# Optimization experiments

Hardware: AMD Instinct MI355X
Metric: run time of the kernel (lower is better)

The kernel has to match this reference:

```python
import jax, jax.numpy as jnp
import numpy as np

N_NODES = 100000
N_EDGES = 600000
EMB_DIM = 128
N_BOND_FEATS = 3
BOND_VOCAB = 8


def setup_inputs() -> dict:
    key = jax.random.key(0)
    k1, k2, k3, k4, k5, k6 = jax.random.split(key, 6)
    h = jax.random.normal(k1, (N_NODES, EMB_DIM), dtype=jnp.float32)
    edge_feat = jax.random.randint(k2, (N_EDGES, N_BOND_FEATS), 0, 5, dtype=jnp.int64)
    dst = jax.random.randint(k3, (N_EDGES,), 0, N_NODES, dtype=jnp.int64)
    bond_emb = jax.random.normal(k4, (N_BOND_FEATS, BOND_VOCAB, EMB_DIM), dtype=jnp.float32)
    W = jax.random.normal(k5, (EMB_DIM, EMB_DIM), dtype=jnp.float32) / jnp.sqrt(jnp.float32(EMB_DIM))
    b = jax.random.normal(k6, (EMB_DIM,), dtype=jnp.float32) * 0.01
    return {"h": h, "edge_feat": edge_feat, "dst": dst, "bond_emb": bond_emb, "W": W, "b": b}


def reference(h, edge_feat, dst, bond_emb, W, b):
    # BondEncoder: sum of per-column embedding lookups -> [E, D]
    # bond_emb[f, edge_feat[:, f]] for each feature column f, summed.
    he = bond_emb[jnp.arange(N_BOND_FEATS)[None, :], edge_feat].sum(axis=1)  # [E, D]
    # fn.v_mul_e: message = dst-node feature * encoded edge feature
    m = h[dst] * he  # [E, D]
    # fn.sum: segment-sum messages onto destination nodes
    agg = jax.ops.segment_sum(m, dst, num_segments=N_NODES)  # [N, D]
    # final Linear(emb_dim, emb_dim)
    return agg @ W.T + b
```

## Files before the change

### kernel.cpp

```cpp
#include <hip/hip_runtime.h>

#define NN 100000
#define NE 600000
#define D 128
#define CW 16

#define OFF_CNTBF  6400000
#define OFF_WSPLIT 9600000
#define OFF_EFRAG  9665536

typedef __attribute__((ext_vector_type(8))) short bf16x8;
typedef __attribute__((ext_vector_type(4))) float f32x4;

__device__ __forceinline__ unsigned short f2bf(float x) {
    unsigned u = __float_as_uint(x);
    u += 0x7FFFu + ((u >> 16) & 1u);
    return (unsigned short)(u >> 16);
}
__device__ __forceinline__ float bf2f(unsigned short s) {
    return __uint_as_float(((unsigned)s) << 16);
}
__device__ __forceinline__ unsigned pack2(unsigned short a, unsigned short b) {
    return (unsigned)a | ((unsigned)b << 16);
}

__global__ __launch_bounds__(256) void prep_kernel(const float* __restrict__ W,
                                                   const float* __restrict__ emb,
                                                   unsigned char* __restrict__ ws) {
    int bid = blockIdx.x;
    if (bid < 1563) {
        int c = bid * 256 + threadIdx.x;
        if (c < 400000) reinterpret_cast<int4*>(ws)[c] = make_int4(0, 0, 0, 0);
    } else if (bid < 1627) {
        int idx = (bid - 1563) * 256 + threadIdx.x;
        float w = W[idx];
        unsigned short hi = f2bf(w);
        unsigned short lo = f2bf(w - bf2f(hi));
        unsigned short* wsplit = (unsigned short*)(ws + OFF_WSPLIT);
        wsplit[idx] = hi;
        wsplit[16384 + idx] = lo;
    } else {
        int i = (bid - 1627) * 256 + threadIdx.x;
        int e = i & 7, l = (i >> 3) & 63, t = (i >> 9) & 7;
        int r = l & 15, lg = l >> 4;
        int j = lg * 8 + e;
        int d = 32 * (t >> 1) + 8 * (r >> 2) + 4 * (t & 1) + (r & 3);
        float v = 0.0f;
        if (j < 15) v = emb[((j / 5) * 8 + (j % 5)) * D + d];
        unsigned short hi = f2bf(v);
        unsigned short lo = f2bf(v - bf2f(hi));
        unsigned short* ef = (unsigned short*)(ws + OFF_EFRAG);
        ef[i] = hi;
        ef[4096 + i] = lo;
    }
}

__global__ __launch_bounds__(256) void hist_kernel(const int* __restrict__ ef,
                                                   const int* __restrict__ dst,
                                                   unsigned* __restrict__ counts) {
    int g = blockIdx.x * 256 + threadIdx.x;
    if (g >= NE / 4) return;
    int4 d4 = reinterpret_cast<const int4*>(dst)[g];
    int4 f0 = reinterpret_cast<const int4*>(ef)[g * 3 + 0];
    int4 f1 = reinterpret_cast<const int4*>(ef)[g * 3 + 1];
    int4 f2 = reinterpret_cast<const int4*>(ef)[g * 3 + 2];
    int fa[12] = {f0.x, f0.y, f0.z, f0.w, f1.x, f1.y, f1.z, f1.w,
                  f2.x, f2.y, f2.z, f2.w};
    int dd[4] = {d4.x, d4.y, d4.z, d4.w};
    #pragma unroll
    for (int i = 0; i < 4; ++i) {
        int combo = fa[i * 3] * 25 + fa[i * 3 + 1] * 5 + fa[i * 3 + 2];
        atomicAdd(counts + dd[i] * CW + (combo >> 3), 1u << ((combo & 7) * 4));
    }
}

__global__ __launch_bounds__(256) void expand_kernel(const unsigned* __restrict__ counts,
                                                     unsigned short* __restrict__ cntbf) {
    int n = blockIdx.x * 256 + threadIdx.x;
    if (n >= NN) return;
    const unsigned* row = counts + n * CW;
    unsigned wd[16];
    #pragma unroll
    for (int i = 0; i < 4; ++i) {
        uint4 v = reinterpret_cast<const uint4*>(row)[i];
        wd[i * 4] = v.x; wd[i * 4 + 1] = v.y; wd[i * 4 + 2] = v.z; wd[i * 4 + 3] = v.w;
    }
    int mi[15];
    #pragma unroll
    for (int j = 0; j < 15; ++j) mi[j] = 0;
    #pragma unroll
    for (int c = 0; c < 125; ++c) {
        int cnt = (int)((wd[c >> 3] >> ((c & 7) * 4)) & 0xFu);
        mi[c / 25] += cnt;
        mi[5 + (c / 5) % 5] += cnt;
        mi[10 + c % 5] += cnt;
    }
    unsigned short o[16];
    #pragma unroll
    for (int j = 0; j < 15; ++j) o[j] = f2bf((float)mi[j]);
    o[15] = 0;
    uint4 u;
    u.x = pack2(o[0], o[1]);   u.y = pack2(o[2], o[3]);
    u.z = pack2(o[4], o[5]);   u.w = pack2(o[6], o[7]);
    reinterpret_cast<uint4*>(cntbf + n * 16)[0] = u;
    u.x = pack2(o[8], o[9]);   u.y = pack2(o[10], o[11]);
    u.z = pack2(o[12], o[13]); u.w = pack2(o[14], o[15]);
    reinterpret_cast<uint4*>(cntbf + n * 16)[1] = u;
}

__global__ __launch_bounds__(512, 4) void fused_kernel(
        const float* __restrict__ h,
        const unsigned short* __restrict__ cntbf,
        const unsigned short* __restrict__ efrag,
        const unsigned short* __restrict__ wsplit,
        const float* __restrict__ b,
        float* __restrict__ out) {
    __shared__ unsigned short sW[2][128 * 128];
    __shared__ unsigned short sA[64 * 128];

    const int tid  = threadIdx.x;
    const int lane = tid & 63;
    const int w    = tid >> 6;
    const int n0   = blockIdx.x * 64;
    const int lr   = lane & 15;
    const int lg   = lane >> 4;

    char* sWb = (char*)&sW[0][0];
    char* sAb = (char*)&sA[0];

    #pragma unroll
    for (int i = 0; i < 8; ++i) {
        int c  = tid + i * 512;
        int p  = c >> 11;
        int r  = (c >> 4) & 127;
        int kc = c & 15;
        int byte = p * 32768 + r * 256 + ((kc * 16) ^ ((r & 7) << 4));
        *reinterpret_cast<uint4*>(sWb + byte) = reinterpret_cast<const uint4*>(wsplit)[c];
    }

    const int ng   = w & 3;
    const int th   = w >> 2;
    const int node = n0 + ng * 16 + lr;
    const bool valid = node < NN;

    bf16x8 cfrag = {0, 0, 0, 0, 0, 0, 0, 0};
    if (valid && lg < 2)
        cfrag = *reinterpret_cast<const bf16x8*>(cntbf + node * 16 + lg * 8);

    f32x4 s[4];
    #pragma unroll
    for (int ti = 0; ti < 4; ++ti) { f32x4 z = {0, 0, 0, 0}; s[ti] = z; }
    #pragma unroll
    for (int p = 0; p < 2; ++p) {
        #pragma unroll
        for (int ti = 0; ti < 4; ++ti) {
            int t = th * 4 + ti;
            bf16x8 ef = *reinterpret_cast<const bf16x8*>(efrag + p * 4096 + t * 512 + lane * 8);
            s[ti] = __builtin_amdgcn_mfma_f32_16x16x32_bf16(ef, cfrag, s[ti], 0, 0, 0);
        }
    }

    #pragma unroll
    for (int q = 0; q < 2; ++q) {
        const int u = th * 2 + q;
        float hv[8];
        if (valid) {
            float4 h0 = *reinterpret_cast<const float4*>(h + node * D + u * 32 + lg * 8);
            float4 h1 = *reinterpret_cast<const float4*>(h + node * D + u * 32 + lg * 8 + 4);
            hv[0] = h0.x; hv[1] = h0.y; hv[2] = h0.z; hv[3] = h0.w;
            hv[4] = h1.x; hv[5] = h1.y; hv[6] = h1.z; hv[7] = h1.w;
        } else {
            #pragma unroll
            for (int e = 0; e < 8; ++e) hv[e] = 0.0f;
        }
        unsigned short o[8];
        #pragma unroll
        for (int e = 0; e < 8; ++e)
            o[e] = f2bf(hv[e] * s[q * 2 + (e >> 2)][e & 3]);
        uint4 uo;
        uo.x = pack2(o[0], o[1]); uo.y = pack2(o[2], o[3]);
        uo.z = pack2(o[4], o[5]); uo.w = pack2(o[6], o[7]);
        int row  = ng * 16 + lr;
        int byte = row * 256 + ((u * 64 + lg * 16) ^ ((row & 7) << 4));
        *reinterpret_cast<uint4*>(sAb + byte) = uo;
    }
    __syncthreads();

    const int mt = w >> 1;
    const int jc = w & 1;

    f32x4 acc[4];
    #pragma unroll
    for (int jb = 0; jb < 4; ++jb) {
        float bv = b[jc * 64 + jb * 16 + lr];
        f32x4 t = {bv, bv, bv, bv};
        acc[jb] = t;
    }

    const int arow = mt * 16 + lr;
    #pragma unroll
    for (int kk = 0; kk < 4; ++kk) {
        int abyte = arow * 256 + ((kk * 64 + lg * 16) ^ ((arow & 7) << 4));
        bf16x8 av = *reinterpret_cast<const bf16x8*>(sAb + abyte);
        #pragma unroll
        for (int jb = 0; jb < 4; ++jb) {
            int brow  = jc * 64 + jb * 16 + lr;
            int wbyte = brow * 256 + ((kk * 64 + lg * 16) ^ ((brow & 7) << 4));
            bf16x8 whi = *reinterpret_cast<const bf16x8*>(sWb + wbyte);
            bf16x8 wlo = *reinterpret_cast<const bf16x8*>(sWb + 32768 + wbyte);
            acc[jb] = __builtin_amdgcn_mfma_f32_16x16x32_bf16(av, whi, acc[jb], 0, 0, 0);
            acc[jb] = __builtin_amdgcn_mfma_f32_16x16x32_bf16(av, wlo, acc[jb], 0, 0, 0);
        }
    }

    #pragma unroll
    for (int jb = 0; jb < 4; ++jb) {
        int col = jc * 64 + jb * 16 + lr;
        #pragma unroll
        for (int r = 0; r < 4; ++r) {
            int n2 = n0 + mt * 16 + lg * 4 + r;
            if (n2 < NN) out[n2 * D + col] = acc[jb][r];
        }
    }
}

extern "C" void kernel_launch(void* const* d_in, const int* in_sizes, int n_in,
                              void* d_out, int out_size, void* d_ws, size_t ws_size,
                              hipStream_t stream) {
    const float* h   = (const float*)d_in[0];
    const int*   ef  = (const int*)d_in[1];
    const int*   dst = (const int*)d_in[2];
    const float* emb = (const float*)d_in[3];
    const float* W   = (const float*)d_in[4];
    const float* b   = (const float*)d_in[5];
    float*       out = (float*)d_out;

    unsigned char*  ws     = (unsigned char*)d_ws;
    unsigned*       counts = (unsigned*)ws;
    unsigned short* cntbf  = (unsigned short*)(ws + OFF_CNTBF);
    unsigned short* wsplit = (unsigned short*)(ws + OFF_WSPLIT);
    unsigned short* efr    = (unsigned short*)(ws + OFF_EFRAG);

    prep_kernel<<<1563 + 64 + 16, 256, 0, stream>>>(W, emb, ws);
    hist_kernel<<<(NE / 4 + 255) / 256, 256, 0, stream>>>(ef, dst, counts);
    expand_kernel<<<(NN + 255) / 256, 256, 0, stream>>>(counts, cntbf);
    fused_kernel<<<(NN + 63) / 64, 512, 0, stream>>>(h, cntbf, efr, wsplit, b, out);
}
```

Measured before the change: 66.20 us.

## Keep A fragments in registers and give each wave a full 16-node tile

```diff
diff --git a/kernel.cpp b/kernel.cpp
--- a/kernel.cpp
+++ b/kernel.cpp
@@ -116,17 +116,15 @@
         const float* __restrict__ b,
         float* __restrict__ out) {
     __shared__ unsigned short sW[2][128 * 128];
-    __shared__ unsigned short sA[64 * 128];
 
     const int tid  = threadIdx.x;
     const int lane = tid & 63;
     const int w    = tid >> 6;
-    const int n0   = blockIdx.x * 64;
+    const int n0   = blockIdx.x * 128;
     const int lr   = lane & 15;
     const int lg   = lane >> 4;
 
     char* sWb = (char*)&sW[0][0];
-    char* sAb = (char*)&sA[0];
 
     #pragma unroll
     for (int i = 0; i < 8; ++i) {
@@ -138,87 +136,80 @@
         *reinterpret_cast<uint4*>(sWb + byte) = reinterpret_cast<const uint4*>(wsplit)[c];
     }
 
-    const int ng   = w & 3;
-    const int th   = w >> 2;
-    const int node = n0 + ng * 16 + lr;
+    const int node  = n0 + w * 16 + lr;
     const bool valid = node < NN;
+
+    float hv[4][8];
+    #pragma unroll
+    for (int kk = 0; kk < 4; ++kk) {
+        if (valid) {
+            float4 h0 = *reinterpret_cast<const float4*>(h + node * D + kk * 32 + lg * 8);
+            float4 h1 = *reinterpret_cast<const float4*>(h + node * D + kk * 32 + lg * 8 + 4);
+            hv[kk][0] = h0.x; hv[kk][1] = h0.y; hv[kk][2] = h0.z; hv[kk][3] = h0.w;
+            hv[kk][4] = h1.x; hv[kk][5] = h1.y; hv[kk][6] = h1.z; hv[kk][7] = h1.w;
+        } else {
+            #pragma unroll
+            for (int e = 0; e < 8; ++e) hv[kk][e] = 0.0f;
+        }
+    }
 
     bf16x8 cfrag = {0, 0, 0, 0, 0, 0, 0, 0};
     if (valid && lg < 2)
         cfrag = *reinterpret_cast<const bf16x8*>(cntbf + node * 16 + lg * 8);
 
-    f32x4 s[4];
-    #pragma unroll
-    for (int ti = 0; ti < 4; ++ti) { f32x4 z = {0, 0, 0, 0}; s[ti] = z; }
+    f32x4 s[8];
+    #pragma unroll
+    for (int t = 0; t < 8; ++t) { f32x4 z = {0, 0, 0, 0}; s[t] = z; }
     #pragma unroll
     for (int p = 0; p < 2; ++p) {
         #pragma unroll
-        for (int ti = 0; ti < 4; ++ti) {
-            int t = th * 4 + ti;
+        for (int t = 0; t < 8; ++t) {
             bf16x8 ef = *reinterpret_cast<const bf16x8*>(efrag + p * 4096 + t * 512 + lane * 8);
-            s[ti] = __builtin_amdgcn_mfma_f32_16x16x32_bf16(ef, cfrag, s[ti], 0, 0, 0);
-        }
-    }
-
-    #pragma unroll
-    for (int q = 0; q < 2; ++q) {
-        const int u = th * 2 + q;
-        float hv[8];
-        if (valid) {
-            float4 h0 = *reinterpret_cast<const float4*>(h + node * D + u * 32 + lg * 8);
-            float4 h1 = *reinterpret_cast<const float4*>(h + node * D + u * 32 + lg * 8 + 4);
-            hv[0] = h0.x; hv[1] = h0.y; hv[2] = h0.z; hv[3] = h0.w;
-            hv[4] = h1.x; hv[5] = h1.y; hv[6] = h1.z; hv[7] = h1.w;
-        } else {
-            #pragma unroll
-            for (int e = 0; e < 8; ++e) hv[e] = 0.0f;
-        }
+            s[t] = __builtin_amdgcn_mfma_f32_16x16x32_bf16(ef, cfrag, s[t], 0, 0, 0);
+        }
+    }
+
+    bf16x8 afrag[4];
+    #pragma unroll
+    for (int kk = 0; kk < 4; ++kk) {
         unsigned short o[8];
         #pragma unroll
         for (int e = 0; e < 8; ++e)
-            o[e] = f2bf(hv[e] * s[q * 2 + (e >> 2)][e & 3]);
-        uint4 uo;
-        uo.x = pack2(o[0], o[1]); uo.y = pack2(o[2], o[3]);
-        uo.z = pack2(o[4], o[5]); uo.w = pack2(o[6], o[7]);
-        int row  = ng * 16 + lr;
-        int byte = row * 256 + ((u * 64 + lg * 16) ^ ((row & 7) << 4));
-        *reinterpret_cast<uint4*>(sAb + byte) = uo;
+            o[e] = f2bf(hv[kk][e] * s[kk * 2 + (e >> 2)][e & 3]);
+        unsigned uo[4];
+        uo[0] = pack2(o[0], o[1]); uo[1] = pack2(o[2], o[3]);
+        uo[2] = pack2(o[4], o[5]); uo[3] = pack2(o[6], o[7]);
+        afrag[kk] = *reinterpret_cast<bf16x8*>(uo);
     }
     __syncthreads();
 
-    const int mt = w >> 1;
-    const int jc = w & 1;
-
-    f32x4 acc[4];
-    #pragma unroll
-    for (int jb = 0; jb < 4; ++jb) {
-        float bv = b[jc * 64 + jb * 16 + lr];
+    f32x4 acc[8];
+    #pragma unroll
+    for (int jb = 0; jb < 8; ++jb) {
+        float bv = b[jb * 16 + lr];
         f32x4 t = {bv, bv, bv, bv};
         acc[jb] = t;
     }
 
-    const int arow = mt * 16 + lr;
     #pragma unroll
     for (int kk = 0; kk < 4; ++kk) {
-        int abyte = arow * 256 + ((kk * 64 + lg * 16) ^ ((arow & 7) << 4));
-        bf16x8 av = *reinterpret_cast<const bf16x8*>(sAb + abyte);
-        #pragma unroll
-        for (int jb = 0; jb < 4; ++jb) {
-            int brow  = jc * 64 + jb * 16 + lr;
+        #pragma unroll
+        for (int jb = 0; jb < 8; ++jb) {
+            int brow  = jb * 16 + lr;
             int wbyte = brow * 256 + ((kk * 64 + lg * 16) ^ ((brow & 7) << 4));
             bf16x8 whi = *reinterpret_cast<const bf16x8*>(sWb + wbyte);
             bf16x8 wlo = *reinterpret_cast<const bf16x8*>(sWb + 32768 + wbyte);
-            acc[jb] = __builtin_amdgcn_mfma_f32_16x16x32_bf16(av, whi, acc[jb], 0, 0, 0);
-            acc[jb] = __builtin_amdgcn_mfma_f32_16x16x32_bf16(av, wlo, acc[jb], 0, 0, 0);
-        }
-    }
-
-    #pragma unroll
-    for (int jb = 0; jb < 4; ++jb) {
-        int col = jc * 64 + jb * 16 + lr;
+            acc[jb] = __builtin_amdgcn_mfma_f32_16x16x32_bf16(afrag[kk], whi, acc[jb], 0, 0, 0);
+            acc[jb] = __builtin_amdgcn_mfma_f32_16x16x32_bf16(afrag[kk], wlo, acc[jb], 0, 0, 0);
+        }
+    }
+
+    #pragma unroll
+    for (int jb = 0; jb < 8; ++jb) {
+        int col = jb * 16 + lr;
         #pragma unroll
         for (int r = 0; r < 4; ++r) {
-            int n2 = n0 + mt * 16 + lg * 4 + r;
+            int n2 = n0 + w * 16 + lg * 4 + r;
             if (n2 < NN) out[n2 * D + col] = acc[jb][r];
         }
     }
@@ -244,5 +235,5 @@
     prep_kernel<<<1563 + 64 + 16, 256, 0, stream>>>(W, emb, ws);
     hist_kernel<<<(NE / 4 + 255) / 256, 256, 0, stream>>>(ef, dst, counts);
     expand_kernel<<<(NN + 255) / 256, 256, 0, stream>>>(counts, cntbf);
-    fused_kernel<<<(NN + 63) / 64, 512, 0, stream>>>(h, cntbf, efr, wsplit, b, out);
-}
+    fused_kernel<<<(NN + 127) / 128, 512, 0, stream>>>(h, cntbf, efr, wsplit, b, out);
+}
```

Result: faster. 63.53 us (-4.0%).

## Split fused kernel into scaled-h elementwise pass and separate bf16 GEMM

Applied to the files above, without the earlier changes.

```diff
diff --git a/kernel.cpp b/kernel.cpp
--- a/kernel.cpp
+++ b/kernel.cpp
@@ -5,9 +5,9 @@
 #define D 128
 #define CW 16
 
-#define OFF_CNTBF  6400000
-#define OFF_WSPLIT 9600000
-#define OFF_EFRAG  9665536
+#define OFF_CNTF   6400000
+#define OFF_HS     12800000
+#define OFF_WSPLIT 38424576
 
 typedef __attribute__((ext_vector_type(8))) short bf16x8;
 typedef __attribute__((ext_vector_type(4))) float f32x4;
@@ -25,13 +25,12 @@
 }
 
 __global__ __launch_bounds__(256) void prep_kernel(const float* __restrict__ W,
-                                                   const float* __restrict__ emb,
                                                    unsigned char* __restrict__ ws) {
     int bid = blockIdx.x;
     if (bid < 1563) {
         int c = bid * 256 + threadIdx.x;
         if (c < 400000) reinterpret_cast<int4*>(ws)[c] = make_int4(0, 0, 0, 0);
-    } else if (bid < 1627) {
+    } else {
         int idx = (bid - 1563) * 256 + threadIdx.x;
         float w = W[idx];
         unsigned short hi = f2bf(w);
@@ -39,19 +38,6 @@
         unsigned short* wsplit = (unsigned short*)(ws + OFF_WSPLIT);
         wsplit[idx] = hi;
         wsplit[16384 + idx] = lo;
-    } else {
-        int i = (bid - 1627) * 256 + threadIdx.x;
-        int e = i & 7, l = (i >> 3) & 63, t = (i >> 9) & 7;
-        int r = l & 15, lg = l >> 4;
-        int j = lg * 8 + e;
-        int d = 32 * (t >> 1) + 8 * (r >> 2) + 4 * (t & 1) + (r & 3);
-        float v = 0.0f;
-        if (j < 15) v = emb[((j / 5) * 8 + (j % 5)) * D + d];
-        unsigned short hi = f2bf(v);
-        unsigned short lo = f2bf(v - bf2f(hi));
-        unsigned short* ef = (unsigned short*)(ws + OFF_EFRAG);
-        ef[i] = hi;
-        ef[4096 + i] = lo;
     }
 }
 
@@ -75,7 +61,7 @@
 }
 
 __global__ __launch_bounds__(256) void expand_kernel(const unsigned* __restrict__ counts,
-                                                     unsigned short* __restrict__ cntbf) {
+                                                     float* __restrict__ cntf) {
     int n = blockIdx.x * 256 + threadIdx.x;
     if (n >= NN) return;
     const unsigned* row = counts + n * CW;
@@ -95,131 +81,133 @@
         mi[5 + (c / 5) % 5] += cnt;
         mi[10 + c % 5] += cnt;
     }
-    unsigned short o[16];
-    #pragma unroll
-    for (int j = 0; j < 15; ++j) o[j] = f2bf((float)mi[j]);
-    o[15] = 0;
+    float* frow = cntf + n * 16;
+    float4 o;
+    o.x = (float)mi[0];  o.y = (float)mi[1];  o.z = (float)mi[2];  o.w = (float)mi[3];
+    reinterpret_cast<float4*>(frow)[0] = o;
+    o.x = (float)mi[4];  o.y = (float)mi[5];  o.z = (float)mi[6];  o.w = (float)mi[7];
+    reinterpret_cast<float4*>(frow)[1] = o;
+    o.x = (float)mi[8];  o.y = (float)mi[9];  o.z = (float)mi[10]; o.w = (float)mi[11];
+    reinterpret_cast<float4*>(frow)[2] = o;
+    o.x = (float)mi[12]; o.y = (float)mi[13]; o.z = (float)mi[14]; o.w = 0.0f;
+    reinterpret_cast<float4*>(frow)[3] = o;
+}
+
+__global__ __launch_bounds__(256) void hs_kernel(const float* __restrict__ h,
+                                                 const float* __restrict__ cntf,
+                                                 const float* __restrict__ emb,
+                                                 unsigned short* __restrict__ hs) {
+    __shared__ float sE[15 * 128];
+    int t = threadIdx.x;
+    for (int i = t; i < 480; i += 256) {
+        int r = i >> 5, c = i & 31;
+        int f = r / 5, v = r - f * 5;
+        reinterpret_cast<float4*>(sE)[r * 32 + c] =
+            reinterpret_cast<const float4*>(emb + (f * 8 + v) * D)[c];
+    }
+    __syncthreads();
+
+    int gt   = blockIdx.x * 256 + t;
+    int node = gt >> 4;
+    int d0   = (gt & 15) * 8;
+
+    float m[15];
+    #pragma unroll
+    for (int j = 0; j < 15; ++j) m[j] = cntf[node * 16 + j];
+
+    float s[8] = {0, 0, 0, 0, 0, 0, 0, 0};
+    #pragma unroll
+    for (int j = 0; j < 15; ++j) {
+        float4 e0 = *reinterpret_cast<const float4*>(&sE[j * 128 + d0]);
+        float4 e1 = *reinterpret_cast<const float4*>(&sE[j * 128 + d0 + 4]);
+        s[0] += m[j] * e0.x;  s[1] += m[j] * e0.y;
+        s[2] += m[j] * e0.z;  s[3] += m[j] * e0.w;
+        s[4] += m[j] * e1.x;  s[5] += m[j] * e1.y;
+        s[6] += m[j] * e1.z;  s[7] += m[j] * e1.w;
+    }
+
+    float4 h0 = *reinterpret_cast<const float4*>(&h[node * D + d0]);
+    float4 h1 = *reinterpret_cast<const float4*>(&h[node * D + d0 + 4]);
+    unsigned short o[8];
+    o[0] = f2bf(h0.x * s[0]); o[1] = f2bf(h0.y * s[1]);
+    o[2] = f2bf(h0.z * s[2]); o[3] = f2bf(h0.w * s[3]);
+    o[4] = f2bf(h1.x * s[4]); o[5] = f2bf(h1.y * s[5]);
+    o[6] = f2bf(h1.z * s[6]); o[7] = f2bf(h1.w * s[7]);
     uint4 u;
-    u.x = pack2(o[0], o[1]);   u.y = pack2(o[2], o[3]);
-    u.z = pack2(o[4], o[5]);   u.w = pack2(o[6], o[7]);
-    reinterpret_cast<uint4*>(cntbf + n * 16)[0] = u;
-    u.x = pack2(o[8], o[9]);   u.y = pack2(o[10], o[11]);
-    u.z = pack2(o[12], o[13]); u.w = pack2(o[14], o[15]);
-    reinterpret_cast<uint4*>(cntbf + n * 16)[1] = u;
-}
-
-__global__ __launch_bounds__(512, 4) void fused_kernel(
-        const float* __restrict__ h,
-        const unsigned short* __restrict__ cntbf,
-        const unsigned short* __restrict__ efrag,
-        const unsigned short* __restrict__ wsplit,
-        const float* __restrict__ b,
-        float* __restrict__ out) {
-    __shared__ unsigned short sW[2][128 * 128];
-    __shared__ unsigned short sA[64 * 128];
-
-    const int tid  = threadIdx.x;
-    const int lane = tid & 63;
-    const int w    = tid >> 6;
-    const int n0   = blockIdx.x * 64;
+    u.x = pack2(o[0], o[1]); u.y = pack2(o[2], o[3]);
+    u.z = pack2(o[4], o[5]); u.w = pack2(o[6], o[7]);
+    *reinterpret_cast<uint4*>(&hs[node * D + d0]) = u;
+}
+
+__global__ __launch_bounds__(512) void gemm_kernel(const unsigned short* __restrict__ hs,
+                                                   const unsigned short* __restrict__ wsplit,
+                                                   const float* __restrict__ bias,
+                                                   float* __restrict__ out) {
+    __shared__ unsigned short sW[2][64 * 128];
+    __shared__ unsigned short sA[128 * 128];
+
+    const int bid  = blockIdx.x;
+    const int n0   = (bid >> 1) * 128;
+    const int c0   = (bid & 1) * 64;
+    const int t    = threadIdx.x;
+    const int lane = t & 63;
+    const int w    = t >> 6;
     const int lr   = lane & 15;
     const int lg   = lane >> 4;
-
-    char* sWb = (char*)&sW[0][0];
-    char* sAb = (char*)&sA[0];
-
-    #pragma unroll
-    for (int i = 0; i < 8; ++i) {
-        int c  = tid + i * 512;
-        int p  = c >> 11;
-        int r  = (c >> 4) & 127;
+    char* sWb = (char*)sW;
+    char* sAb = (char*)sA;
+
+    #pragma unroll
+    for (int i = 0; i < 4; ++i) {
+        int c  = t + i * 512;
+        int p  = c >> 10;
+        int r  = (c >> 4) & 63;
         int kc = c & 15;
-        int byte = p * 32768 + r * 256 + ((kc * 16) ^ ((r & 7) << 4));
-        *reinterpret_cast<uint4*>(sWb + byte) = reinterpret_cast<const uint4*>(wsplit)[c];
-    }
-
-    const int ng   = w & 3;
-    const int th   = w >> 2;
-    const int node = n0 + ng * 16 + lr;
-    const bool valid = node < NN;
-
-    bf16x8 cfrag = {0, 0, 0, 0, 0, 0, 0, 0};
-    if (valid && lg < 2)
-        cfrag = *reinterpret_cast<const bf16x8*>(cntbf + node * 16 + lg * 8);
-
-    f32x4 s[4];
-    #pragma unroll
-    for (int ti = 0; ti < 4; ++ti) { f32x4 z = {0, 0, 0, 0}; s[ti] = z; }
-    #pragma unroll
-    for (int p = 0; p < 2; ++p) {
-        #pragma unroll
-        for (int ti = 0; ti < 4; ++ti) {
-            int t = th * 4 + ti;
-            bf16x8 ef = *reinterpret_cast<const bf16x8*>(efrag + p * 4096 + t * 512 + lane * 8);
-            s[ti] = __builtin_amdgcn_mfma_f32_16x16x32_bf16(ef, cfrag, s[ti], 0, 0, 0);
-        }
-    }
-
-    #pragma unroll
-    for (int q = 0; q < 2; ++q) {
-        const int u = th * 2 + q;
-        float hv[8];
-        if (valid) {
-            float4 h0 = *reinterpret_cast<const float4*>(h + node * D + u * 32 + lg * 8);
-            float4 h1 = *reinterpret_cast<const float4*>(h + node * D + u * 32 + lg * 8 + 4);
-            hv[0] = h0.x; hv[1] = h0.y; hv[2] = h0.z; hv[3] = h0.w;
-            hv[4] = h1.x; hv[5] = h1.y; hv[6] = h1.z; hv[7] = h1.w;
-        } else {
-            #pragma unroll
-            for (int e = 0; e < 8; ++e) hv[e] = 0.0f;
-        }
-        unsigned short o[8];
-        #pragma unroll
-        for (int e = 0; e < 8; ++e)
-            o[e] = f2bf(hv[e] * s[q * 2 + (e >> 2)][e & 3]);
-        uint4 uo;
-        uo.x = pack2(o[0], o[1]); uo.y = pack2(o[2], o[3]);
-        uo.z = pack2(o[4], o[5]); uo.w = pack2(o[6], o[7]);
-        int row  = ng * 16 + lr;
-        int byte = row * 256 + ((u * 64 + lg * 16) ^ ((row & 7) << 4));
-        *reinterpret_cast<uint4*>(sAb + byte) = uo;
+        uint4 v = *reinterpret_cast<const uint4*>(wsplit + p * 16384 + (c0 + r) * 128 + kc * 8);
+        int byte = p * 16384 + r * 256 + ((kc * 16) ^ ((r & 7) << 4));
+        *reinterpret_cast<uint4*>(sWb + byte) = v;
+    }
+    #pragma unroll
+    for (int i = 0; i < 4; ++i) {
+        int c   = t + i * 512;
+        int row = c >> 4, kc = c & 15;
+        uint4 v = *reinterpret_cast<const uint4*>(hs + n0 * D + c * 8);
+        int byte = row * 256 + ((kc * 16) ^ ((row & 7) << 4));
+        *reinterpret_cast<uint4*>(sAb + byte) = v;
     }
     __syncthreads();
 
-    const int mt = w >> 1;
-    const int jc = w & 1;
-
     f32x4 acc[4];
     #pragma unroll
     for (int jb = 0; jb < 4; ++jb) {
-        float bv = b[jc * 64 + jb * 16 + lr];
-        f32x4 t = {bv, bv, bv, bv};
-        acc[jb] = t;
-    }
-
-    const int arow = mt * 16 + lr;
+        float bv = bias[c0 + jb * 16 + lr];
+        f32x4 tt = {bv, bv, bv, bv};
+        acc[jb] = tt;
+    }
+
+    const int arow = w * 16 + lr;
     #pragma unroll
     for (int kk = 0; kk < 4; ++kk) {
         int abyte = arow * 256 + ((kk * 64 + lg * 16) ^ ((arow & 7) << 4));
         bf16x8 av = *reinterpret_cast<const bf16x8*>(sAb + abyte);
         #pragma unroll
         for (int jb = 0; jb < 4; ++jb) {
-            int brow  = jc * 64 + jb * 16 + lr;
+            int brow  = jb * 16 + lr;
             int wbyte = brow * 256 + ((kk * 64 + lg * 16) ^ ((brow & 7) << 4));
-            bf16x8 whi = *reinterpret_cast<const bf16x8*>(sWb + wbyte);
-            bf16x8 wlo = *reinterpret_cast<const bf16x8*>(sWb + 32768 + wbyte);
-            acc[jb] = __builtin_amdgcn_mfma_f32_16x16x32_bf16(av, whi, acc[jb], 0, 0, 0);
-            acc[jb] = __builtin_amdgcn_mfma_f32_16x16x32_bf16(av, wlo, acc[jb], 0, 0, 0);
+            bf16x8 wh = *reinterpret_cast<const bf16x8*>(sWb + wbyte);
+            bf16x8 wl = *reinterpret_cast<const bf16x8*>(sWb + 16384 + wbyte);
+            acc[jb] = __builtin_amdgcn_mfma_f32_16x16x32_bf16(av, wh, acc[jb], 0, 0, 0);
+            acc[jb] = __builtin_amdgcn_mfma_f32_16x16x32_bf16(av, wl, acc[jb], 0, 0, 0);
         }
     }
 
     #pragma unroll
     for (int jb = 0; jb < 4; ++jb) {
-        int col = jc * 64 + jb * 16 + lr;
+        int col = c0 + jb * 16 + lr;
         #pragma unroll
         for (int r = 0; r < 4; ++r) {
-            int n2 = n0 + mt * 16 + lg * 4 + r;
-            if (n2 < NN) out[n2 * D + col] = acc[jb][r];
+            int node = n0 + w * 16 + lg * 4 + r;
+            if (node < NN) out[node * D + col] = acc[jb][r];
         }
     }
 }
@@ -237,12 +225,13 @@
 
     unsigned char*  ws     = (unsigned char*)d_ws;
     unsigned*       counts = (unsigned*)ws;
-    unsigned short* cntbf  = (unsigned short*)(ws + OFF_CNTBF);
+    float*          cntf   = (float*)(ws + OFF_CNTF);
+    unsigned short* hs     = (unsigned short*)(ws + OFF_HS);
     unsigned short* wsplit = (unsigned short*)(ws + OFF_WSPLIT);
-    unsigned short* efr    = (unsigned short*)(ws + OFF_EFRAG);
-
-    prep_kernel<<<1563 + 64 + 16, 256, 0, stream>>>(W, emb, ws);
+
+    prep_kernel<<<1563 + 64, 256, 0, stream>>>(W, ws);
     hist_kernel<<<(NE / 4 + 255) / 256, 256, 0, stream>>>(ef, dst, counts);
-    expand_kernel<<<(NN + 255) / 256, 256, 0, stream>>>(counts, cntbf);
-    fused_kernel<<<(NN + 63) / 64, 512, 0, stream>>>(h, cntbf, efr, wsplit, b, out);
-}
+    expand_kernel<<<(NN + 255) / 256, 256, 0, stream>>>(counts, cntf);
+    hs_kernel<<<NN * 16 / 256, 256, 0, stream>>>(h, cntf, emb, hs);
+    gemm_kernel<<<((NN + 127) / 128) * 2, 512, 0, stream>>>(hs, wsplit, b, out);
+}
```

After: 75.20 us. +13.6%, slower.
